# Performance work log

Measured on AMD Instinct MI355X. Metric: run time of the kernel, lower is better.

## Reference

```python
import jax, jax.numpy as jnp
import numpy as np

B, NU, IN, H, VD = 4096, 6, 600, 600, 400
KD_IN, NH_IN = 64, 1
KD_C, NH_C = 32, 4
K = 4


def setup_inputs() -> dict:
    key = jax.random.key(0)
    ks = jax.random.split(key, 12)
    f = jax.random.normal
    return dict(
        x=f(ks[0], (B, 1, IN), jnp.float32),
        hs=f(ks[1], (B, NU, H), jnp.float32),
        cs=f(ks[2], (B, NU, H), jnp.float32),
        Wk=f(ks[3], (IN, NH_IN * KD_IN), jnp.float32) * 0.02,   # input-attn key Linear (no bias)
        Wv=f(ks[4], (IN, NH_IN * VD), jnp.float32) * 0.02,      # input-attn value Linear (no bias)
        Wq=f(ks[5], (NU, H, NH_IN * KD_IN), jnp.float32) * 0.01,  # GroupLinear query
        Wi2h=f(ks[6], (NU, VD, 4 * H), jnp.float32) * 0.01,     # GroupLSTMCell i2h
        Wh2h=f(ks[7], (NU, H, 4 * H), jnp.float32) * 0.01,      # GroupLSTMCell h2h
        Wck=f(ks[8], (NU, H, NH_C * KD_C), jnp.float32) * 0.01,  # comm key GroupLinear
        Wcq=f(ks[9], (NU, H, NH_C * KD_C), jnp.float32) * 0.01,  # comm query GroupLinear
        Wcv=f(ks[10], (NU, H, NH_C * H), jnp.float32) * 0.01,   # comm value GroupLinear
        Wco=f(ks[11], (NU, NH_C * H, H), jnp.float32) * 0.01,   # comm output_fc GroupLinear
    )


def _heads(t, nh, d):
    # (B, N, nh*d) -> (B, nh, N, d)
    b, n, _ = t.shape
    return t.reshape(b, n, nh, d).transpose(0, 2, 1, 3)


def reference(x, hs, cs, Wk, Wv, Wq, Wi2h, Wh2h, Wck, Wcq, Wcv, Wco):
    b = x.shape[0]
    # append null input along key axis -> (B, 2, IN)
    xcat = jnp.concatenate([x, jnp.zeros((b, 1, IN), x.dtype)], axis=1)

    # ---- input attention + top-k unit mask ----
    key = _heads(xcat @ Wk, NH_IN, KD_IN)                 # (B, nh, 2, kd)
    val = _heads(xcat @ Wv, NH_IN, VD).mean(axis=1)       # (B, 2, vd) (mean over heads)
    qry = _heads(jnp.einsum('buh,uhk->buk', hs, Wq), NH_IN, KD_IN)  # (B, nh, NU, kd)
    scores = jnp.einsum('bhuk,bhmk->bhum', qry, key) / jnp.sqrt(jnp.asarray(KD_IN, x.dtype))
    scores = scores.mean(axis=1)                          # (B, NU, 2)
    idx = jax.lax.top_k(scores[:, :, 0], K)[1]            # (B, K) active units
    mask = jnp.zeros((b, NU), x.dtype).at[jnp.arange(b)[:, None], idx].set(1.0)
    probs = jax.nn.softmax(scores, axis=-1)               # (dropout p is identity in eval)
    inputs = jnp.einsum('bum,bmv->buv', probs, val) * mask[:, :, None]  # (B, NU, vd)

    # ---- grouped LSTM cell ----
    preact = (jnp.einsum('buv,uvo->buo', inputs, Wi2h)
              + jnp.einsum('buh,uho->buo', hs, Wh2h))     # (B, NU, 4H)
    gates = jax.nn.sigmoid(preact[:, :, :3 * H])
    g_t = jnp.tanh(preact[:, :, 3 * H:])
    i_t = gates[:, :, :H]
    f_t = gates[:, :, H:2 * H]
    o_t = gates[:, :, 2 * H:]
    c_t = cs * f_t + i_t * g_t
    h_t = o_t * jnp.tanh(c_t)

    # ---- blocked_grad: identity fwd, grad*mask bwd ----
    m3 = mask[:, :, None]
    h_b = h_t * m3 + jax.lax.stop_gradient(h_t * (1.0 - m3))

    # ---- masked communication attention ----
    ck = _heads(jnp.einsum('buh,uhk->buk', h_b, Wck), NH_C, KD_C)  # (B, nh, NU, kd)
    cq = _heads(jnp.einsum('buh,uhk->buk', h_b, Wcq), NH_C, KD_C)
    cv = _heads(jnp.einsum('buh,uhk->buk', h_b, Wcv), NH_C, H)     # (B, nh, NU, H)
    cscores = jnp.einsum('bhuk,bhmk->bhum', cq, ck) / jnp.sqrt(jnp.asarray(KD_C, x.dtype))
    cprobs = jax.nn.softmax(cscores, axis=-1) * mask[:, None, :, None]  # mask query rows
    ctx = jnp.einsum('bhum,bhmd->bhud', cprobs, cv)       # (B, nh, NU, H)
    ctx = ctx.transpose(0, 2, 1, 3).reshape(b, NU, NH_C * H)
    ctx = jnp.einsum('buf,ufo->buo', ctx, Wco)            # (B, NU, H)
    h_new = ctx + h_b

    # ---- keep inactive units' old state ----
    hs_out = m3 * h_new + (1.0 - m3) * hs
    cs_out = m3 * c_t + (1.0 - m3) * cs
    return hs_out, cs_out
```

## Files before the change

### kernel.cpp

```cpp
#include <hip/hip_runtime.h>
#include <cstdint>
#include <cstddef>


typedef _Float16 f16;
typedef _Float16 f16x8 __attribute__((ext_vector_type(8)));
typedef float    f32x4 __attribute__((ext_vector_type(4)));

__device__ __forceinline__ void async16(const void* g, void* l) {
    __builtin_amdgcn_global_load_lds((const __attribute__((address_space(1))) void*)g,
                                     (__attribute__((address_space(3))) void*)l,
                                     16, 0, 0);
}

template <typename CT>
__global__ __launch_bounds__(256)
void mfma_gemm(const f16* __restrict__ A, const f16* __restrict__ W,
               CT* __restrict__ C, int K, int lda, int ldc,
               long sAu, long sWu, long sCu)
{
    A += (long)blockIdx.z * sAu;
    W += (long)blockIdx.z * sWu;
    C += (long)blockIdx.z * sCu;
    const int tm = blockIdx.x * 128;
    const int tn = blockIdx.y * 128;
    __shared__ __attribute__((aligned(16))) f16 As[2][128 * 64];
    __shared__ __attribute__((aligned(16))) f16 Ws[2][128 * 64];
    const int tid  = threadIdx.x;
    const int wave = tid >> 6;
    const int lane = tid & 63;
    const int wm = (wave >> 1) * 64;
    const int wn = (wave & 1) * 64;
    const int srow = lane >> 3;
    const int scol = ((lane & 7) ^ srow) * 8;
    const int mrow = lane & 15;
    const int kq   = (lane >> 4) * 8;
    const int swz  = (mrow & 7) << 3;

    f32x4 acc[4][4] = {};

    auto stage = [&](int b, int kk) {
#pragma unroll
        for (int t = 0; t < 4; t++) {
            const int rbase = t * 32 + wave * 8;
            async16(A + (long)(tm + rbase + srow) * lda + (kk + scol), &As[b][rbase * 64]);
            async16(W + (long)(tn + rbase + srow) * K   + (kk + scol), &Ws[b][rbase * 64]);
        }
    };
    auto compute = [&](int b) {
#pragma unroll
        for (int c = 0; c < 2; c++) {
            const int cc = (c * 32 + kq) ^ swz;
            f16x8 aF[4], wF[4];
#pragma unroll
            for (int i = 0; i < 4; i++)
                aF[i] = *(const f16x8*)&As[b][(wm + i * 16 + mrow) * 64 + cc];
#pragma unroll
            for (int j = 0; j < 4; j++)
                wF[j] = *(const f16x8*)&Ws[b][(wn + j * 16 + mrow) * 64 + cc];
#pragma unroll
            for (int i = 0; i < 4; i++)
#pragma unroll
                for (int j = 0; j < 4; j++)
                    acc[i][j] = __builtin_amdgcn_mfma_f32_16x16x32_f16(aF[i], wF[j], acc[i][j], 0, 0, 0);
        }
    };

    stage(0, 0);
    int bsel = 0;
    const int nk = K >> 6;
    for (int s = 0; s < nk; s++) {
        __syncthreads();
        if (s + 1 < nk) stage(bsel ^ 1, (s + 1) << 6);
        compute(bsel);
        bsel ^= 1;
    }
    const int rrow = (lane >> 4) * 4;
#pragma unroll
    for (int i = 0; i < 4; i++)
#pragma unroll
        for (int j = 0; j < 4; j++)
#pragma unroll
            for (int r = 0; r < 4; r++)
                C[(long)(tm + wm + i * 16 + rrow + r) * ldc + (tn + wn + j * 16 + mrow)] = (CT)acc[i][j][r];
}

__global__ __launch_bounds__(256)
void sgemm_fused(const float* __restrict__ hs, const float* __restrict__ Wq,
                 const float* __restrict__ x, const float* __restrict__ Wk,
                 float* __restrict__ q, float* __restrict__ kx)
{
    const int z = blockIdx.z;
    const float* A; const float* W; float* C; int lda, ldc;
    if (z < 6) { A = hs + z * 600; W = Wq + (long)z * 38400; C = q + z * 64; lda = 3600; ldc = 384; }
    else       { A = x;            W = Wk;                   C = kx;         lda = 600;  ldc = 64;  }
    const int K = 600;
    const int tm = blockIdx.x * 64;
    __shared__ __attribute__((aligned(16))) float AsT[16][64];
    __shared__ __attribute__((aligned(16))) float Ws[16][64];
    const int t = threadIdx.x;
    const int arow = t >> 2, akc = (t & 3) * 4;
    const int wkw = t >> 4, wn = (t & 15) * 4;
    const int tx = t & 15, ty = t >> 4;

    float4 aR, wR;
    const float* Arow = A + (long)(tm + arow) * lda;
    auto loadA = [&](int kk) {
        const int k0 = kk + akc;
        const float* p = Arow + k0;
        if (k0 + 3 < K) aR = *(const float4*)p;
        else {
            aR.x = (k0 + 0 < K) ? p[0] : 0.f; aR.y = (k0 + 1 < K) ? p[1] : 0.f;
            aR.z = (k0 + 2 < K) ? p[2] : 0.f; aR.w = (k0 + 3 < K) ? p[3] : 0.f;
        }
    };
    auto loadW = [&](int kk) {
        const int k = kk + wkw;
        if (k < K) wR = *(const float4*)(W + (long)k * 64 + wn);
        else       wR = float4{0.f, 0.f, 0.f, 0.f};
    };
    loadA(0); loadW(0);
    float acc[4][4] = {{0.f}};
    const int NS = 38;
    for (int s = 0; s < NS; s++) {
        __syncthreads();
        AsT[akc + 0][arow] = aR.x; AsT[akc + 1][arow] = aR.y;
        AsT[akc + 2][arow] = aR.z; AsT[akc + 3][arow] = aR.w;
        *(float4*)&Ws[wkw][wn] = wR;
        __syncthreads();
        if (s + 1 < NS) { loadA((s + 1) * 16); loadW((s + 1) * 16); }
#pragma unroll
        for (int k = 0; k < 16; k++) {
            const float4 av = *(const float4*)&AsT[k][ty * 4];
            const float4 wv = *(const float4*)&Ws[k][tx * 4];
            acc[0][0] += av.x * wv.x; acc[0][1] += av.x * wv.y; acc[0][2] += av.x * wv.z; acc[0][3] += av.x * wv.w;
            acc[1][0] += av.y * wv.x; acc[1][1] += av.y * wv.y; acc[1][2] += av.y * wv.z; acc[1][3] += av.y * wv.w;
            acc[2][0] += av.z * wv.x; acc[2][1] += av.z * wv.y; acc[2][2] += av.z * wv.z; acc[2][3] += av.z * wv.w;
            acc[3][0] += av.w * wv.x; acc[3][1] += av.w * wv.y; acc[3][2] += av.w * wv.z; acc[3][3] += av.w * wv.w;
        }
    }
#pragma unroll
    for (int r = 0; r < 4; r++)
#pragma unroll
        for (int c = 0; c < 4; c++)
            C[(long)(tm + ty * 4 + r) * ldc + tx * 4 + c] = acc[r][c];
}

__global__ __launch_bounds__(256)
void wtrans(const float* __restrict__ src, f16* __restrict__ dst,
            int K, int N, int Kp, int Np, int ldd, long sSrc, long sDst)
{
    src += (long)blockIdx.z * sSrc;
    dst += (long)blockIdx.z * sDst;
    __shared__ float tile[32][33];
    const int tK = blockIdx.x * 32, tN = blockIdx.y * 32;
    const int tx = threadIdx.x & 31, ty = threadIdx.x >> 5;
#pragma unroll
    for (int i = 0; i < 4; i++) {
        const int k = tK + ty + i * 8, n = tN + tx;
        tile[ty + i * 8][tx] = (k < K && n < N) ? src[(long)k * N + n] : 0.f;
    }
    __syncthreads();
#pragma unroll
    for (int i = 0; i < 4; i++) {
        const int n = tN + ty + i * 8, k = tK + tx;
        if (n < Np && k < Kp) dst[(long)n * ldd + k] = (f16)tile[tx][ty + i * 8];
    }
}

__global__ void xconv_kernel(const float* __restrict__ x, f16* __restrict__ xf, long n)
{
    const long i = (long)blockIdx.x * 256 + threadIdx.x;
    if (i >= n) return;
    const long b = i / 640;
    const int c = (int)(i - b * 640);
    xf[i] = (f16)(c < 600 ? x[b * 600 + c] : 0.f);
}

__global__ void s0_kernel(const float* __restrict__ q, const float* __restrict__ kx,
                          float* __restrict__ s0, int n)
{
    const int i = blockIdx.x * 256 + threadIdx.x;
    if (i >= n) return;
    const int b = i / 6;
    const float* qp = q + (long)i * 64;
    const float* kp = kx + (long)b * 64;
    float s = 0.f;
#pragma unroll
    for (int k = 0; k < 64; k++) s += qp[k] * kp[k];
    s0[i] = s * 0.125f;
}

__global__ void mask_kernel(const float* __restrict__ s0, float* __restrict__ mask,
                            float* __restrict__ alpha, int Bc)
{
    const int b = blockIdx.x * 256 + threadIdx.x;
    if (b >= Bc) return;
    float v[6];
#pragma unroll
    for (int u = 0; u < 6; u++) v[u] = s0[b * 6 + u];
#pragma unroll
    for (int u = 0; u < 6; u++) {
        int rank = 0;
#pragma unroll
        for (int m = 0; m < 6; m++)
            rank += ((v[m] > v[u]) || (v[m] == v[u] && m < u)) ? 1 : 0;
        const float mk = (rank < 4) ? 1.f : 0.f;
        mask[b * 6 + u] = mk;
        alpha[b * 6 + u] = mk / (1.f + __expf(-v[u]));
    }
}

__global__ void inputs_kernel(const float* __restrict__ vx, const float* __restrict__ hs,
                              const float* __restrict__ alpha, f16* __restrict__ icat, long n)
{
    const long i = (long)blockIdx.x * 256 + threadIdx.x;
    if (i >= n) return;
    const int k = (int)(i & 1023);
    const long bu = i >> 10;
    float v;
    if (k < 400)       v = alpha[bu] * vx[(bu / 6) * 512 + k];
    else if (k < 1000) v = hs[bu * 600 + (k - 400)];
    else               v = 0.f;
    icat[i] = (f16)v;
}

__device__ __forceinline__ float tanh_fast(float x) {
    x = fminf(20.f, fmaxf(-20.f, x));
    const float e = __expf(2.f * x);
    return (e - 1.f) / (e + 1.f);
}

__global__ void lstm_kernel(const f16* __restrict__ pre, const float* __restrict__ cs,
                            const float* __restrict__ mask, float* __restrict__ cs_out,
                            f16* __restrict__ hbf, long n)
{
    const long i = (long)blockIdx.x * 256 + threadIdx.x;
    if (i >= n) return;
    const long bu = i / 640;
    const int h = (int)(i - bu * 640);
    if (h >= 600) { hbf[i] = (f16)0.f; return; }
    const f16* p = pre + bu * 2432;
    const float ig = 1.f / (1.f + __expf(-(float)p[h]));
    const float fg = 1.f / (1.f + __expf(-(float)p[600 + h]));
    const float og = 1.f / (1.f + __expf(-(float)p[1200 + h]));
    const float g  = tanh_fast((float)p[1800 + h]);
    const float cold = cs[bu * 600 + h];
    const float c = cold * fg + ig * g;
    cs_out[bu * 600 + h] = (mask[bu] != 0.f) ? c : cold;
    hbf[i] = (f16)(og * tanh_fast(c));
}

__global__ __launch_bounds__(256)
void attn_kernel(const f16* __restrict__ out2, const float* __restrict__ mask,
                 f16* __restrict__ ctx)
{
    const long b = blockIdx.x;
    __shared__ float sck[6][128];
    __shared__ float scq[6][128];
    __shared__ float sp[4][6][6];
    const int t = threadIdx.x;
#pragma unroll
    for (int m = 0; m < 6; m++) {
        const f16* row = out2 + (b * 6 + m) * 2688;
        if (t < 128) sck[m][t] = (float)row[2400 + t];
        else         scq[m][t - 128] = (float)row[2528 + (t - 128)];
    }
    __syncthreads();
    if (t < 144) {
        const int h = t / 36, u = (t / 6) % 6, m = t % 6;
        float s = 0.f;
#pragma unroll
        for (int k = 0; k < 32; k++) s += scq[u][h * 32 + k] * sck[m][h * 32 + k];
        sp[h][u][m] = s * 0.1767766952966369f;
    }
    __syncthreads();
    if (t < 24) {
        const int h = t / 6, u = t % 6;
        float mx = sp[h][u][0];
#pragma unroll
        for (int m = 1; m < 6; m++) mx = fmaxf(mx, sp[h][u][m]);
        float e[6], sum = 0.f;
#pragma unroll
        for (int m = 0; m < 6; m++) { e[m] = __expf(sp[h][u][m] - mx); sum += e[m]; }
        const float sc = mask[b * 6 + u] / sum;
#pragma unroll
        for (int m = 0; m < 6; m++) sp[h][u][m] = e[m] * sc;
    }
    __syncthreads();
    for (int f = t; f < 2432; f += 256) {
        if (f < 2400) {
            const int h = f / 600;
            float cv[6];
#pragma unroll
            for (int m = 0; m < 6; m++) cv[m] = (float)out2[(b * 6 + m) * 2688 + f];
#pragma unroll
            for (int u = 0; u < 6; u++) {
                float s = 0.f;
#pragma unroll
                for (int m = 0; m < 6; m++) s += sp[h][u][m] * cv[m];
                ctx[(b * 6 + u) * 2432 + f] = (f16)s;
            }
        } else {
#pragma unroll
            for (int u = 0; u < 6; u++) ctx[(b * 6 + u) * 2432 + f] = (f16)0.f;
        }
    }
}

__global__ void epi_kernel(const f16* __restrict__ ctxW, const f16* __restrict__ hbf,
                           const float* __restrict__ hs, const float* __restrict__ mask,
                           float* __restrict__ hs_out, long n)
{
    const long i = (long)blockIdx.x * 256 + threadIdx.x;
    if (i >= n) return;
    const long bu = i / 600;
    const int h = (int)(i - bu * 600);
    hs_out[i] = (mask[bu] != 0.f) ? ((float)ctxW[bu * 640 + h] + (float)hbf[bu * 640 + h]) : hs[i];
}

static inline unsigned cdivu(long a, long b) { return (unsigned)((a + b - 1) / b); }

extern "C" void kernel_launch(void* const* d_in, const int* in_sizes, int n_in,
                              void* d_out, int out_size, void* d_ws, size_t ws_size,
                              hipStream_t stream)
{
    (void)in_sizes; (void)n_in; (void)out_size;
    const float* x    = (const float*)d_in[0];
    const float* hs   = (const float*)d_in[1];
    const float* cs   = (const float*)d_in[2];
    const float* Wk   = (const float*)d_in[3];
    const float* Wv   = (const float*)d_in[4];
    const float* Wq   = (const float*)d_in[5];
    const float* Wi2h = (const float*)d_in[6];
    const float* Wh2h = (const float*)d_in[7];
    const float* Wck  = (const float*)d_in[8];
    const float* Wcq  = (const float*)d_in[9];
    const float* Wcv  = (const float*)d_in[10];
    const float* Wco  = (const float*)d_in[11];
    float* hs_out = (float*)d_out;
    float* cs_out = hs_out + (long)4096 * 6 * 600;

    char* wsb = (char*)d_ws;
    size_t off = 0;
    auto alloc = [&](size_t bytes) -> char* {
        char* p = wsb + off;
        off += (bytes + 255) & ~(size_t)255;
        return p;
    };

    f16* W1T = (f16*)alloc((size_t)6 * 2432 * 1024 * 2);
    f16* W2T = (f16*)alloc((size_t)6 * 2688 * 640 * 2);
    f16* W3T = (f16*)alloc((size_t)6 * 640 * 2432 * 2);
    f16* WvT = (f16*)alloc((size_t)512 * 640 * 2);

    f16*   xf   = (f16*)  alloc((size_t)4096 * 640 * 2);
    float* kx   = (float*)alloc((size_t)4096 * 64 * 4);
    float* vx   = (float*)alloc((size_t)4096 * 512 * 4);
    float* q    = (float*)alloc((size_t)4096 * 384 * 4);
    float* s0   = (float*)alloc((size_t)4096 * 6 * 4);
    float* alph = (float*)alloc((size_t)4096 * 6 * 4);
    float* mskv = (float*)alloc((size_t)4096 * 6 * 4);
    const size_t fixedbytes = off;

    const size_t perRow = 81408;
    int Bc = 4096;
    while (Bc > 128 && fixedbytes + (size_t)Bc * perRow + 16384 > ws_size) Bc >>= 1;

    f16* icat = (f16*)alloc((size_t)Bc * 6 * 1024 * 2);
    f16* pre  = (f16*)alloc((size_t)Bc * 6 * 2432 * 2);
    f16* hbf  = (f16*)alloc((size_t)Bc * 6 * 640 * 2);
    f16* out2 = (f16*)alloc((size_t)Bc * 6 * 2688 * 2);
    f16* ctx  = pre;
    f16* ctxW = out2;

    wtrans<<<dim3(13, 76, 6), 256, 0, stream>>>(Wi2h, W1T,        400, 2400, 400, 2432, 1024, 960000L,  2490368L);
    wtrans<<<dim3(20, 76, 6), 256, 0, stream>>>(Wh2h, W1T + 400,  600, 2400, 624, 2432, 1024, 1440000L, 2490368L);
    wtrans<<<dim3(20, 75, 6), 256, 0, stream>>>(Wcv,  W2T,        600, 2400, 640, 2400, 640,  1440000L, 1720320L);
    wtrans<<<dim3(20, 4, 6),  256, 0, stream>>>(Wck,  W2T + (long)2400 * 640, 600, 128, 640, 128, 640, 76800L, 1720320L);
    wtrans<<<dim3(20, 5, 6),  256, 0, stream>>>(Wcq,  W2T + (long)2528 * 640, 600, 128, 640, 160, 640, 76800L, 1720320L);
    wtrans<<<dim3(76, 20, 6), 256, 0, stream>>>(Wco,  W3T,        2400, 600, 2432, 640, 2432, 1440000L, 1556480L);
    wtrans<<<dim3(20, 16, 1), 256, 0, stream>>>(Wv,   WvT,        600,  400, 640, 512, 640,  0L, 0L);

    xconv_kernel<<<cdivu((long)4096 * 640, 256), 256, 0, stream>>>(x, xf, (long)4096 * 640);
    sgemm_fused<<<dim3(64, 1, 7), 256, 0, stream>>>(hs, Wq, x, Wk, q, kx);
    mfma_gemm<float><<<dim3(32, 4, 1), 256, 0, stream>>>(xf, WvT, vx, 640, 640, 512, 0, 0, 0);
    s0_kernel<<<cdivu((long)4096 * 6, 256), 256, 0, stream>>>(q, kx, s0, 4096 * 6);
    mask_kernel<<<cdivu(4096, 256), 256, 0, stream>>>(s0, mskv, alph, 4096);

    for (int b0 = 0; b0 < 4096; b0 += Bc) {
        const float* hsc = hs + (long)b0 * 3600;
        const float* csc = cs + (long)b0 * 3600;
        float* hso = hs_out + (long)b0 * 3600;
        float* cso = cs_out + (long)b0 * 3600;

        inputs_kernel<<<cdivu((long)Bc * 6144, 256), 256, 0, stream>>>(
            vx + (long)b0 * 512, hsc, alph + (long)b0 * 6, icat, (long)Bc * 6144);
        mfma_gemm<f16><<<dim3(Bc / 128, 19, 6), 256, 0, stream>>>(icat, W1T, pre, 1024, 6144, 14592, 1024, 2490368, 2432);
        lstm_kernel<<<cdivu((long)Bc * 3840, 256), 256, 0, stream>>>(
            pre, csc, mskv + (long)b0 * 6, cso, hbf, (long)Bc * 3840);
        mfma_gemm<f16><<<dim3(Bc / 128, 21, 6), 256, 0, stream>>>(hbf, W2T, out2, 640, 3840, 16128, 640, 1720320, 2688);
        attn_kernel<<<Bc, 256, 0, stream>>>(out2, mskv + (long)b0 * 6, ctx);
        mfma_gemm<f16><<<dim3(Bc / 128, 5, 6), 256, 0, stream>>>(ctx, W3T, ctxW, 2432, 14592, 3840, 2432, 1556480, 640);
        epi_kernel<<<cdivu((long)Bc * 3600, 256), 256, 0, stream>>>(
            ctxW, hbf, hsc, mskv + (long)b0 * 6, hso, (long)Bc * 3600);
    }
}
```

Before: 1.027 ms.

## Use larger 256-row MFMA GEMM tiles with 512 threads and XCD-aware block remap

Adds a new MFMA GEMM kernel with 256xBN tiles, 8 waves per block and a block-id remap that spreads consecutive tiles across the 8 XCDs. It pads the transposed weight buffers to multiples of 256 columns and guards stores with a real-N bound. The three grouped GEMMs switch to it to raise per-block data reuse and cut global and LDS traffic per FLOP. The cost is more LDS and register pressure, which may lower occupancy, and some padded work in the N dimension.

New measurement: 1.030 ms. Within noise of the previous version (+0.3%).

```diff
diff --git a/kernel.cpp b/kernel.cpp
--- a/kernel.cpp
+++ b/kernel.cpp
@@ -11,6 +11,97 @@
     __builtin_amdgcn_global_load_lds((const __attribute__((address_space(1))) void*)g,
                                      (__attribute__((address_space(3))) void*)l,
                                      16, 0, 0);
+}
+
+template <typename CT, int BN, int WM, int WN>
+__global__ __launch_bounds__(512, 2)
+void mfma_gemm2(const f16* __restrict__ A, const f16* __restrict__ W,
+                CT* __restrict__ C, int K, int lda, int ldc, int Nreal,
+                long sAu, long sWu, long sCu)
+{
+    constexpr int MI = 256 / WM / 16;
+    const int gx = gridDim.x, gy = gridDim.y;
+    int bid = blockIdx.x + gx * (blockIdx.y + gy * blockIdx.z);
+    const int nwg = gx * gy * gridDim.z;
+    if ((nwg & 7) == 0)
+        bid = (bid & 7) * (nwg >> 3) + (bid >> 3);
+    const int bx  = bid % gx;
+    const int byz = bid / gx;
+    const int by  = byz % gy;
+    const int bz  = byz / gy;
+    A += (long)bz * sAu;
+    W += (long)bz * sWu;
+    C += (long)bz * sCu;
+    const int tm = bx * 256;
+    const int tn = by * BN;
+
+    __shared__ __attribute__((aligned(16))) f16 As[2][256 * 64];
+    __shared__ __attribute__((aligned(16))) f16 Ws[2][BN * 64];
+
+    const int tid  = threadIdx.x;
+    const int wave = tid >> 6;
+    const int lane = tid & 63;
+    const int wm = (wave / WN) * (256 / WM);
+    const int wn = (wave % WN) * (BN / WN);
+    const int srow = lane >> 3;
+    const int scol = ((lane & 7) ^ srow) * 8;
+    const int mrow = lane & 15;
+    const int kq   = (lane >> 4) * 8;
+    const int swz  = (mrow & 7) << 3;
+
+    f32x4 acc[MI][4] = {};
+
+    auto stage = [&](int b, int kk) {
+#pragma unroll
+        for (int t = 0; t < 4; t++) {
+            const int rb = t * 64 + wave * 8;
+            async16(A + (long)(tm + rb + srow) * lda + (kk + scol), &As[b][rb * 64]);
+        }
+#pragma unroll
+        for (int t = 0; t < BN / 64; t++) {
+            const int rb = t * 64 + wave * 8;
+            async16(W + (long)(tn + rb + srow) * K + (kk + scol), &Ws[b][rb * 64]);
+        }
+    };
+    auto compute = [&](int b) {
+#pragma unroll
+        for (int c = 0; c < 2; c++) {
+            const int cc = (c * 32 + kq) ^ swz;
+            f16x8 aF[MI], wF[4];
+#pragma unroll
+            for (int i = 0; i < MI; i++)
+                aF[i] = *(const f16x8*)&As[b][(wm + i * 16 + mrow) * 64 + cc];
+#pragma unroll
+            for (int j = 0; j < 4; j++)
+                wF[j] = *(const f16x8*)&Ws[b][(wn + j * 16 + mrow) * 64 + cc];
+#pragma unroll
+            for (int i = 0; i < MI; i++)
+#pragma unroll
+                for (int j = 0; j < 4; j++)
+                    acc[i][j] = __builtin_amdgcn_mfma_f32_16x16x32_f16(aF[i], wF[j], acc[i][j], 0, 0, 0);
+        }
+    };
+
+    stage(0, 0);
+    int bsel = 0;
+    const int nk = K >> 6;
+    for (int s = 0; s < nk; s++) {
+        __syncthreads();
+        if (s + 1 < nk) stage(bsel ^ 1, (s + 1) << 6);
+        compute(bsel);
+        bsel ^= 1;
+    }
+    const int rrow = (lane >> 4) * 4;
+#pragma unroll
+    for (int i = 0; i < MI; i++)
+#pragma unroll
+        for (int j = 0; j < 4; j++) {
+            const int col = tn + wn + j * 16 + mrow;
+            if (col < Nreal)
+#pragma unroll
+                for (int r = 0; r < 4; r++)
+                    C[(long)(tm + wm + i * 16 + rrow + r) * ldc + col] = (CT)acc[i][j][r];
+        }
 }
 
 template <typename CT>
@@ -349,8 +440,8 @@
         return p;
     };
 
-    f16* W1T = (f16*)alloc((size_t)6 * 2432 * 1024 * 2);
-    f16* W2T = (f16*)alloc((size_t)6 * 2688 * 640 * 2);
+    f16* W1T = (f16*)alloc((size_t)6 * 2560 * 1024 * 2);
+    f16* W2T = (f16*)alloc((size_t)6 * 2816 * 640 * 2);
     f16* W3T = (f16*)alloc((size_t)6 * 640 * 2432 * 2);
     f16* WvT = (f16*)alloc((size_t)512 * 640 * 2);
 
@@ -365,7 +456,7 @@
 
     const size_t perRow = 81408;
     int Bc = 4096;
-    while (Bc > 128 && fixedbytes + (size_t)Bc * perRow + 16384 > ws_size) Bc >>= 1;
+    while (Bc > 256 && fixedbytes + (size_t)Bc * perRow + 16384 > ws_size) Bc >>= 1;
 
     f16* icat = (f16*)alloc((size_t)Bc * 6 * 1024 * 2);
     f16* pre  = (f16*)alloc((size_t)Bc * 6 * 2432 * 2);
@@ -374,11 +465,11 @@
     f16* ctx  = pre;
     f16* ctxW = out2;
 
-    wtrans<<<dim3(13, 76, 6), 256, 0, stream>>>(Wi2h, W1T,        400, 2400, 400, 2432, 1024, 960000L,  2490368L);
-    wtrans<<<dim3(20, 76, 6), 256, 0, stream>>>(Wh2h, W1T + 400,  600, 2400, 624, 2432, 1024, 1440000L, 2490368L);
-    wtrans<<<dim3(20, 75, 6), 256, 0, stream>>>(Wcv,  W2T,        600, 2400, 640, 2400, 640,  1440000L, 1720320L);
-    wtrans<<<dim3(20, 4, 6),  256, 0, stream>>>(Wck,  W2T + (long)2400 * 640, 600, 128, 640, 128, 640, 76800L, 1720320L);
-    wtrans<<<dim3(20, 5, 6),  256, 0, stream>>>(Wcq,  W2T + (long)2528 * 640, 600, 128, 640, 160, 640, 76800L, 1720320L);
+    wtrans<<<dim3(13, 80, 6), 256, 0, stream>>>(Wi2h, W1T,        400, 2400, 400, 2560, 1024, 960000L,  2621440L);
+    wtrans<<<dim3(20, 80, 6), 256, 0, stream>>>(Wh2h, W1T + 400,  600, 2400, 624, 2560, 1024, 1440000L, 2621440L);
+    wtrans<<<dim3(20, 75, 6), 256, 0, stream>>>(Wcv,  W2T,        600, 2400, 640, 2400, 640,  1440000L, 1802240L);
+    wtrans<<<dim3(20, 4, 6),  256, 0, stream>>>(Wck,  W2T + (long)2400 * 640, 600, 128, 640, 128, 640, 76800L, 1802240L);
+    wtrans<<<dim3(20, 9, 6),  256, 0, stream>>>(Wcq,  W2T + (long)2528 * 640, 600, 128, 640, 288, 640, 76800L, 1802240L);
     wtrans<<<dim3(76, 20, 6), 256, 0, stream>>>(Wco,  W3T,        2400, 600, 2432, 640, 2432, 1440000L, 1556480L);
     wtrans<<<dim3(20, 16, 1), 256, 0, stream>>>(Wv,   WvT,        600,  400, 640, 512, 640,  0L, 0L);
 
@@ -396,12 +487,15 @@
 
         inputs_kernel<<<cdivu((long)Bc * 6144, 256), 256, 0, stream>>>(
             vx + (long)b0 * 512, hsc, alph + (long)b0 * 6, icat, (long)Bc * 6144);
-        mfma_gemm<f16><<<dim3(Bc / 128, 19, 6), 256, 0, stream>>>(icat, W1T, pre, 1024, 6144, 14592, 1024, 2490368, 2432);
+        mfma_gemm2<f16, 256, 2, 4><<<dim3(Bc / 256, 10, 6), 512, 0, stream>>>(
+            icat, W1T, pre, 1024, 6144, 14592, 2432, 1024, 2621440, 2432);
         lstm_kernel<<<cdivu((long)Bc * 3840, 256), 256, 0, stream>>>(
             pre, csc, mskv + (long)b0 * 6, cso, hbf, (long)Bc * 3840);
-        mfma_gemm<f16><<<dim3(Bc / 128, 21, 6), 256, 0, stream>>>(hbf, W2T, out2, 640, 3840, 16128, 640, 1720320, 2688);
+        mfma_gemm2<f16, 256, 2, 4><<<dim3(Bc / 256, 11, 6), 512, 0, stream>>>(
+            hbf, W2T, out2, 640, 3840, 16128, 2688, 640, 1802240, 2688);
         attn_kernel<<<Bc, 256, 0, stream>>>(out2, mskv + (long)b0 * 6, ctx);
-        mfma_gemm<f16><<<dim3(Bc / 128, 5, 6), 256, 0, stream>>>(ctx, W3T, ctxW, 2432, 14592, 3840, 2432, 1556480, 640);
+        mfma_gemm2<f16, 128, 4, 2><<<dim3(Bc / 256, 5, 6), 512, 0, stream>>>(
+            ctx, W3T, ctxW, 2432, 14592, 3840, 640, 2432, 1556480, 640);
         epi_kernel<<<cdivu((long)Bc * 3600, 256), 256, 0, stream>>>(
             ctxW, hbf, hsc, mskv + (long)b0 * 6, hso, (long)Bc * 3600);
     }
```
